# Optimization experiments

Measured on AMD Instinct MI355X. Metric: run time of the kernel, lower is better.

## Reference

```python
import jax, jax.numpy as jnp
import numpy as np

INPUT_DIM = 4096
BOTTLENECK = 32768
A = 2
K = 0.05
# eval-mode sparsity count: max(1, int(bottleneck * a * k))
K_COUNT = max(1, int(BOTTLENECK * A * K))  # 3276


def setup_inputs() -> dict:
    key = jax.random.key(0)
    kx, kw = jax.random.split(key)
    x = jax.random.normal(kx, (4096, INPUT_DIM), dtype=jnp.float32)
    # encoder weight [bottleneck, input_dim], like nn.Linear(input_dim, bottleneck)
    W = jax.random.normal(kw, (BOTTLENECK, INPUT_DIM), dtype=jnp.float32) * (1.0 / np.sqrt(INPUT_DIM))
    b_enc = jnp.zeros((BOTTLENECK,), dtype=jnp.float32)
    b_dec = jnp.zeros((INPUT_DIM,), dtype=jnp.float32)
    return {"x": x, "W": W, "b_enc": b_enc, "b_dec": b_dec, "epoch": 0}


def reference(x, W, b_enc, b_dec, epoch):
    # encode: z1 = x @ W^T + b_enc  -> [B, bottleneck]
    z1 = jnp.einsum("bi,hi->bh", x, W) + b_enc
    # eval-mode k-winner-take-all mask over dim 1
    _, topk_idx = jax.lax.top_k(z1, K_COUNT)  # [B, K_COUNT]
    rows = jnp.arange(z1.shape[0])[:, None]
    mask = jnp.zeros_like(z1).at[rows, topk_idx].set(1.0)
    a1 = z1 * mask
    # tied-weight decode: z2 = a1 @ W + b_dec -> [B, input_dim]
    z2 = jnp.einsum("bh,hi->bi", a1, W) + b_dec
    return z2
```

## Files before the change

### kernel.cpp

```cpp
#include <hip/hip_runtime.h>
#include <hip/hip_bf16.h>
#include <stdint.h>


#define DIM      4096
#define BATCH    4096
#define NROWS_W  32768
#define KCNT     3276
#define DELTA    0.0066f
#define ROWCAP   256
#define HCAP     64
#define CANDCAP  3584

typedef __bf16 bf16x8 __attribute__((ext_vector_type(8)));
typedef __bf16 bf16x4 __attribute__((ext_vector_type(4)));
typedef float  f32x4  __attribute__((ext_vector_type(4)));

__device__ __forceinline__ void gload_lds16(const void* g, void* l) {
  __builtin_amdgcn_global_load_lds(
      (const __attribute__((address_space(1))) void*)g,
      (__attribute__((address_space(3))) void*)l, 16, 0, 0);
}

__global__ void k_cvtx(const float* __restrict__ s, __bf16* __restrict__ hi, int n4) {
  int i = blockIdx.x * 256 + threadIdx.x;
  const int stride = gridDim.x * 256;
  for (; i < n4; i += stride) {
    f32x4 v = ((const f32x4*)s)[i];
    bf16x4 h;
#pragma unroll
    for (int j = 0; j < 4; ++j) h[j] = (__bf16)v[j];
    ((bf16x4*)hi)[i] = h;
  }
}

__global__ void k_splitw(const float* __restrict__ W, __bf16* __restrict__ Wh,
                         __bf16* __restrict__ Wt) {
  __shared__ __bf16 t[64][65];
  const int c0 = blockIdx.x * 64, r0 = blockIdx.y * 64;
  const int tx = threadIdx.x, ty = threadIdx.y;
  for (int rr = ty; rr < 64; rr += 8) {
    const float w = W[(long)(r0 + rr) * DIM + c0 + tx];
    const __bf16 h = (__bf16)w;
    Wh[(long)(r0 + rr) * DIM + c0 + tx] = h;
    t[rr][tx] = h;
  }
  __syncthreads();
  for (int cc = ty; cc < 64; cc += 8)
    Wt[(long)(c0 + cc) * NROWS_W + r0 + tx] = t[tx][cc];
}

__global__ __launch_bounds__(256, 2)
void k_gemm(const __bf16* __restrict__ A, const __bf16* __restrict__ B,
            const float* __restrict__ bias, float* __restrict__ C,
            int M, int N, int Kt) {
  constexpr int BM = 128, BN = 128, BK = 64;
  __shared__ __align__(16) __bf16 sA[BM * BK];
  __shared__ __align__(16) __bf16 sB[BN * BK];

  const int tid = threadIdx.x;
  const int nbn = N / BN;
  int bm, bn;
  if ((M / BM) % 16 == 0 && nbn % 32 == 0) {
    const int nsbn = nbn / 32;
    const int g = blockIdx.x >> 9, r = blockIdx.x & 511;
    bm = (g / nsbn) * 16 + (r >> 5);
    bn = (g % nsbn) * 32 + (r & 31);
  } else {
    bm = blockIdx.x / nbn;
    bn = blockIdx.x % nbn;
  }
  const int m0 = bm * BM, n0 = bn * BN;
  const int lane = tid & 63, wid = tid >> 6;
  const int wm = wid >> 1, wn = wid & 1;
  const int lr = lane & 15, lk = lane >> 4;
  const int swz = (lr & 7) << 4;

  f32x4 acc[4][4] = {};

  for (int k0 = 0; k0 < Kt; k0 += BK) {
#pragma unroll
    for (int r = 0; r < 4; ++r) {
      const int o = (r * 256 + tid) * 16;
      const int row = o >> 7;
      const int colb = (o & 127) ^ ((row & 7) << 4);
      const long gA = ((long)(m0 + row) * Kt + k0) * 2 + colb;
      const long gB = ((long)(n0 + row) * Kt + k0) * 2 + colb;
      gload_lds16((const char*)A + gA, (char*)sA + o);
      gload_lds16((const char*)B + gB, (char*)sB + o);
    }
    __syncthreads();

#pragma unroll
    for (int kk = 0; kk < 2; ++kk) {
      bf16x8 va[4], vb[4];
      const int kbase = (kk * 64 + lk * 16) ^ swz;
#pragma unroll
      for (int m = 0; m < 4; ++m) {
        const int row = wm * 64 + m * 16 + lr;
        va[m] = *(const bf16x8*)((const char*)sA + row * 128 + kbase);
      }
#pragma unroll
      for (int n = 0; n < 4; ++n) {
        const int row = wn * 64 + n * 16 + lr;
        vb[n] = *(const bf16x8*)((const char*)sB + row * 128 + kbase);
      }
#pragma unroll
      for (int m = 0; m < 4; ++m)
#pragma unroll
        for (int n = 0; n < 4; ++n)
          acc[m][n] = __builtin_amdgcn_mfma_f32_16x16x32_bf16(va[m], vb[n], acc[m][n], 0, 0, 0);
    }
    __syncthreads();
  }

#pragma unroll
  for (int n = 0; n < 4; ++n) {
    const int col = n0 + wn * 64 + n * 16 + lr;
    const float bv = bias[col];
#pragma unroll
    for (int m = 0; m < 4; ++m) {
      const int r0r = m0 + wm * 64 + m * 16 + lk * 4;
#pragma unroll
      for (int j = 0; j < 4; ++j)
        C[(long)(r0r + j) * N + col] = acc[m][n][j] + bv;
    }
  }
}

__device__ __forceinline__ unsigned f2o(float f) {
  unsigned b = __float_as_uint(f);
  return ((int)b < 0) ? ~b : (b | 0x80000000u);
}
__device__ __forceinline__ float o2f(unsigned u) {
  unsigned b = (u & 0x80000000u) ? (u & 0x7FFFFFFFu) : ~u;
  return __uint_as_float(b);
}

__global__ __launch_bounds__(256)
void k_topk4(const float* __restrict__ z1, float* __restrict__ thr,
             unsigned* __restrict__ rowlist, unsigned* __restrict__ rowcnt,
             unsigned* __restrict__ c1, unsigned* __restrict__ bucket,
             unsigned* __restrict__ bcnt, __bf16* __restrict__ a1, int kwant) {
  __shared__ unsigned hist[4096];
  __shared__ float cv[CANDCAP];
  __shared__ unsigned short ci[CANDCAP];
  __shared__ unsigned s_n, s_bin, s_rem, s_wt[4], s_cnt, s_above;
  const int tid = threadIdx.x;
  const int b = blockIdx.x;
  const f32x4* zv = (const f32x4*)(z1 + (long)b * NROWS_W);
  constexpr int NV = NROWS_W / 4;

#pragma unroll
  for (int j = 0; j < 16; ++j) hist[tid + j * 256] = 0;
  if (tid == 0) { s_n = 0; s_cnt = 0; s_above = 0; }
  __syncthreads();
  for (int i = tid; i < NV; i += 256) {
    f32x4 v = zv[i];
#pragma unroll
    for (int j = 0; j < 4; ++j) atomicAdd(&hist[f2o(v[j]) >> 20], 1u);
  }
  __syncthreads();
  unsigned p = 0;
#pragma unroll
  for (int j = 0; j < 16; ++j) p += hist[tid * 16 + j];
  unsigned sfx = p;
  const int lane = tid & 63, w = tid >> 6;
#pragma unroll
  for (int off = 1; off < 64; off <<= 1) {
    unsigned o = __shfl_down(sfx, off);
    sfx += (lane + off < 64) ? o : 0u;
  }
  if (lane == 0) s_wt[w] = sfx;
  __syncthreads();
  unsigned above_waves = 0;
  for (int ww = w + 1; ww < 4; ++ww) above_waves += s_wt[ww];
  const unsigned incl = sfx + above_waves;
  const int cnt = __syncthreads_count(incl >= (unsigned)kwant);
  const int tstar = cnt - 1;
  if (tid == tstar) {
    unsigned cum = incl - p;
    int bsel = tid * 16;
    for (int j = 15; j >= 0; --j) {
      const unsigned h = hist[tid * 16 + j];
      if (cum + h >= (unsigned)kwant) { bsel = tid * 16 + j; break; }
      cum += h;
    }
    s_bin = (unsigned)bsel;
    s_rem = (unsigned)kwant - cum;
  }
  __syncthreads();
  const unsigned binsel = s_bin;
  unsigned rem = s_rem;

  const unsigned blo = (binsel > 0) ? binsel - 1 : 0;
  const unsigned bhi = (binsel < 4095) ? binsel + 1 : 4095;
  for (int i = tid; i < NV; i += 256) {
    f32x4 v = zv[i];
#pragma unroll
    for (int j = 0; j < 4; ++j) {
      const unsigned bin = f2o(v[j]) >> 20;
      if (bin >= blo && bin <= bhi) {
        const unsigned jj = atomicAdd(&s_n, 1u);
        if (jj < CANDCAP) { cv[jj] = v[j]; ci[jj] = (unsigned short)(i * 4 + j); }
      }
    }
  }
  __syncthreads();
  const int n = (s_n < CANDCAP) ? (int)s_n : CANDCAP;

  unsigned pfx = 0;
#pragma unroll
  for (int pass = 0; pass < 3; ++pass) {
    const int shift = (pass == 0) ? 12 : (pass == 1) ? 4 : 0;
    const int nb = (pass == 2) ? 16 : 256;
    if (tid < 256) hist[tid] = 0;
    __syncthreads();
    for (int i = tid; i < n; i += 256) {
      const unsigned u = f2o(cv[i]);
      if ((u >> 20) != binsel) continue;
      const unsigned v = u & 0xFFFFFu;
      const bool m = (pass == 0) ? true
                     : (pass == 1) ? ((v >> 12) == (pfx >> 12))
                                   : ((v >> 4) == (pfx >> 4));
      if (m) atomicAdd(&hist[(v >> shift) & (nb - 1)], 1u);
    }
    __syncthreads();
    if (tid == 0) {
      unsigned cum = 0;
      int d = nb - 1;
      for (; d > 0; --d) {
        if (cum + hist[d] >= rem) break;
        cum += hist[d];
      }
      s_bin = (unsigned)d;
      s_rem = rem - cum;
    }
    __syncthreads();
    pfx |= (s_bin << shift);
    rem = s_rem;
    __syncthreads();
  }
  const float t = o2f((binsel << 20) | pfx);
  if (tid == 0) thr[b] = t;
  const float hi = t + DELTA, lo = t - DELTA;

  for (int i = tid; i < n; i += 256) {
    const float v = cv[i];
    if (v >= lo && v <= hi) {
      const unsigned idx = ci[i];
      const unsigned jj = atomicAdd(&s_cnt, 1u);
      if (jj < ROWCAP) {
        rowlist[(long)b * ROWCAP + jj] = idx;
        const unsigned pq = atomicAdd(&bcnt[idx], 1u);
        if (pq < HCAP) bucket[(long)idx * HCAP + pq] = ((unsigned)b << 9) | jj;
      }
    }
  }

  unsigned my_above = 0;
  bf16x4* av = (bf16x4*)(a1 + (long)b * NROWS_W);
  for (int i = tid; i < NV; i += 256) {
    f32x4 v = zv[i];
    bf16x4 o;
#pragma unroll
    for (int j = 0; j < 4; ++j) {
      const bool in = v[j] > hi;
      my_above += in ? 1u : 0u;
      o[j] = in ? (__bf16)v[j] : (__bf16)0.0f;
    }
    av[i] = o;
  }
  atomicAdd(&s_above, my_above);
  __syncthreads();
  if (tid == 0) {
    rowcnt[b] = (s_cnt < ROWCAP) ? s_cnt : ROWCAP;
    c1[b] = s_above;
  }
}

__global__ void k_zero(f32x4* __restrict__ p, int nvec) {
  int i = blockIdx.x * 256 + threadIdx.x;
  if (i < nvec) {
    f32x4 z = {0.f, 0.f, 0.f, 0.f};
    p[i] = z;
  }
}

__global__ void k_recompute(const float* __restrict__ W, const float* __restrict__ x,
                            const unsigned* __restrict__ bucket,
                            const unsigned* __restrict__ bcnt,
                            float* __restrict__ exact) {
  const int h = blockIdx.x;
  unsigned n = bcnt[h];
  if (n > HCAP) n = HCAP;
  if (n == 0) return;
  __shared__ float wrec[DIM];
  const long wb = (long)h * DIM;
  for (int i = threadIdx.x; i < DIM / 4; i += 256)
    ((f32x4*)wrec)[i] = ((const f32x4*)(W + wb))[i];
  __syncthreads();
  const int w = threadIdx.x >> 6, lane = threadIdx.x & 63;
  for (unsigned e = w; e < n; e += 4) {
    const unsigned ent = bucket[(long)h * HCAP + e];
    const int b = ent >> 9, j = ent & 511;
    const f32x4* xv = (const f32x4*)(x + (long)b * DIM);
    float s = 0.f;
#pragma unroll
    for (int c = 0; c < 16; ++c) {
      const int i4 = c * 64 + lane;
      f32x4 v = xv[i4];
      const float* wr = &wrec[i4 * 4];
#pragma unroll
      for (int q = 0; q < 4; ++q) s += v[q] * wr[q];
    }
#pragma unroll
    for (int m = 32; m; m >>= 1) s += __shfl_xor(s, m);
    if (lane == 0) exact[(long)b * ROWCAP + j] = s;
  }
}

__global__ void k_select(const float* __restrict__ exact, const unsigned* __restrict__ rowlist,
                         const unsigned* __restrict__ rowcnt, const unsigned* __restrict__ c1,
                         const float* __restrict__ z1, __bf16* __restrict__ a1) {
  const int b = blockIdx.x;
  const int n = (int)rowcnt[b];
  const int need = KCNT - (int)c1[b];
  __shared__ float vals[ROWCAP];
  const int j = threadIdx.x;
  vals[j] = (j < n) ? exact[(long)b * ROWCAP + j] : -1e30f;
  __syncthreads();
  if (j < n) {
    const float vj = vals[j];
    int rank = 0;
    for (int i = 0; i < n; ++i) {
      const float vi = vals[i];
      rank += (vi > vj || (vi == vj && i < j)) ? 1 : 0;
    }
    if (rank < need) {
      const unsigned h = rowlist[(long)b * ROWCAP + j];
      const long off = (long)b * NROWS_W + h;
      a1[off] = (__bf16)z1[off];
    }
  }
}

extern "C" void kernel_launch(void* const* d_in, const int* in_sizes, int n_in,
                              void* d_out, int out_size, void* d_ws, size_t ws_size,
                              hipStream_t stream) {
  const float* x     = (const float*)d_in[0];
  const float* W     = (const float*)d_in[1];
  const float* b_enc = (const float*)d_in[2];
  const float* b_dec = (const float*)d_in[3];
  float* out = (float*)d_out;

  const long NW = (long)NROWS_W * DIM;
  const long NX = (long)BATCH * DIM;
  const long NZ = (long)BATCH * NROWS_W;

  char* ws = (char*)d_ws;
  __bf16* Wh = (__bf16*)ws;
  __bf16* Wt = Wh + NW;
  __bf16* xh = Wt + NW;
  float*  z1 = (float*)(xh + NX);
  float*  thr = z1 + NZ;
  char*   sc = (char*)(thr + BATCH);
  unsigned* rowcnt  = (unsigned*)sc;
  unsigned* c1      = (unsigned*)(sc + 16384);
  unsigned* bcnt    = (unsigned*)(sc + 32768);
  float*    exact   = (float*)(sc + 163840);
  unsigned* rowlist = (unsigned*)(sc + 4358144);
  unsigned* bucket  = (unsigned*)(sc + 8552448);
  __bf16* a1 = Wh;

  const size_t needed = (size_t)(4 * NW + 2 * NX) + (size_t)4 * NZ + 4 * BATCH + 17000000;
  if (ws_size < needed) return;

  k_splitw<<<dim3(DIM / 64, NROWS_W / 64), dim3(64, 8), 0, stream>>>(W, Wh, Wt);
  k_cvtx<<<2048, 256, 0, stream>>>(x, xh, (int)(NX / 4));

  k_gemm<<<(BATCH / 128) * (NROWS_W / 128), 256, 0, stream>>>(
      xh, Wh, b_enc, z1, BATCH, NROWS_W, DIM);

  k_zero<<<32, 256, 0, stream>>>((f32x4*)bcnt, 131072 / 16);
  k_topk4<<<BATCH, 256, 0, stream>>>(z1, thr, rowlist, rowcnt, c1, bucket, bcnt, a1, KCNT);
  k_recompute<<<NROWS_W, 256, 0, stream>>>(W, x, bucket, bcnt, exact);
  k_select<<<BATCH, ROWCAP, 0, stream>>>(exact, rowlist, rowcnt, c1, z1, a1);

  k_gemm<<<(BATCH / 128) * (DIM / 128), 256, 0, stream>>>(
      a1, Wt, b_dec, out, BATCH, DIM, NROWS_W);
}
```

Before: 3.553 ms.

## Switch GEMM operands to fp16, narrow threshold band, fold bcnt zeroing

Converts the x and W copies, the sparse activation and both MFMA GEMMs from bf16 to fp16. fp16 keeps more mantissa bits, so the band of uncertain values around the top-k threshold shrinks from 0.0066 to 0.0025. That means fewer candidates go through the exact fp32 recompute and select kernels. The separate zeroing kernel for bcnt is folded into the weight split kernel, removing one launch. The risk is fp16 overflow or underflow on inputs outside this test's range, and a narrower band could misclassify borderline top-k elements.

```diff
diff --git a/kernel.cpp b/kernel.cpp
--- a/kernel.cpp
+++ b/kernel.cpp
@@ -7,14 +7,14 @@
 #define BATCH    4096
 #define NROWS_W  32768
 #define KCNT     3276
-#define DELTA    0.0066f
+#define DELTA    0.0025f
 #define ROWCAP   256
 #define HCAP     64
 #define CANDCAP  3584
 
-typedef __bf16 bf16x8 __attribute__((ext_vector_type(8)));
-typedef __bf16 bf16x4 __attribute__((ext_vector_type(4)));
-typedef float  f32x4  __attribute__((ext_vector_type(4)));
+typedef _Float16 f16x8 __attribute__((ext_vector_type(8)));
+typedef _Float16 f16x4 __attribute__((ext_vector_type(4)));
+typedef float    f32x4 __attribute__((ext_vector_type(4)));
 
 __device__ __forceinline__ void gload_lds16(const void* g, void* l) {
   __builtin_amdgcn_global_load_lds(
@@ -22,26 +22,33 @@
       (__attribute__((address_space(3))) void*)l, 16, 0, 0);
 }
 
-__global__ void k_cvtx(const float* __restrict__ s, __bf16* __restrict__ hi, int n4) {
+__global__ void k_cvtx(const float* __restrict__ s, _Float16* __restrict__ hi, int n4) {
   int i = blockIdx.x * 256 + threadIdx.x;
   const int stride = gridDim.x * 256;
   for (; i < n4; i += stride) {
     f32x4 v = ((const f32x4*)s)[i];
-    bf16x4 h;
-#pragma unroll
-    for (int j = 0; j < 4; ++j) h[j] = (__bf16)v[j];
-    ((bf16x4*)hi)[i] = h;
-  }
-}
-
-__global__ void k_splitw(const float* __restrict__ W, __bf16* __restrict__ Wh,
-                         __bf16* __restrict__ Wt) {
-  __shared__ __bf16 t[64][65];
+    f16x4 h;
+#pragma unroll
+    for (int j = 0; j < 4; ++j) h[j] = (_Float16)v[j];
+    ((f16x4*)hi)[i] = h;
+  }
+}
+
+__global__ void k_splitw(const float* __restrict__ W, _Float16* __restrict__ Wh,
+                         _Float16* __restrict__ Wt, f32x4* __restrict__ bcntv) {
+  __shared__ _Float16 t[64][65];
   const int c0 = blockIdx.x * 64, r0 = blockIdx.y * 64;
   const int tx = threadIdx.x, ty = threadIdx.y;
+  if (blockIdx.y == 0) {
+    const int idx = blockIdx.x * 512 + ty * 64 + tx;
+    if (idx < 8192) {
+      f32x4 z = {0.f, 0.f, 0.f, 0.f};
+      bcntv[idx] = z;
+    }
+  }
   for (int rr = ty; rr < 64; rr += 8) {
     const float w = W[(long)(r0 + rr) * DIM + c0 + tx];
-    const __bf16 h = (__bf16)w;
+    const _Float16 h = (_Float16)w;
     Wh[(long)(r0 + rr) * DIM + c0 + tx] = h;
     t[rr][tx] = h;
   }
@@ -51,12 +58,12 @@
 }
 
 __global__ __launch_bounds__(256, 2)
-void k_gemm(const __bf16* __restrict__ A, const __bf16* __restrict__ B,
+void k_gemm(const _Float16* __restrict__ A, const _Float16* __restrict__ B,
             const float* __restrict__ bias, float* __restrict__ C,
             int M, int N, int Kt) {
   constexpr int BM = 128, BN = 128, BK = 64;
-  __shared__ __align__(16) __bf16 sA[BM * BK];
-  __shared__ __align__(16) __bf16 sB[BN * BK];
+  __shared__ __align__(16) _Float16 sA[BM * BK];
+  __shared__ __align__(16) _Float16 sB[BN * BK];
 
   const int tid = threadIdx.x;
   const int nbn = N / BN;
@@ -93,23 +100,23 @@
 
 #pragma unroll
     for (int kk = 0; kk < 2; ++kk) {
-      bf16x8 va[4], vb[4];
+      f16x8 va[4], vb[4];
       const int kbase = (kk * 64 + lk * 16) ^ swz;
 #pragma unroll
       for (int m = 0; m < 4; ++m) {
         const int row = wm * 64 + m * 16 + lr;
-        va[m] = *(const bf16x8*)((const char*)sA + row * 128 + kbase);
+        va[m] = *(const f16x8*)((const char*)sA + row * 128 + kbase);
       }
 #pragma unroll
       for (int n = 0; n < 4; ++n) {
         const int row = wn * 64 + n * 16 + lr;
-        vb[n] = *(const bf16x8*)((const char*)sB + row * 128 + kbase);
+        vb[n] = *(const f16x8*)((const char*)sB + row * 128 + kbase);
       }
 #pragma unroll
       for (int m = 0; m < 4; ++m)
 #pragma unroll
         for (int n = 0; n < 4; ++n)
-          acc[m][n] = __builtin_amdgcn_mfma_f32_16x16x32_bf16(va[m], vb[n], acc[m][n], 0, 0, 0);
+          acc[m][n] = __builtin_amdgcn_mfma_f32_16x16x32_f16(va[m], vb[n], acc[m][n], 0, 0, 0);
     }
     __syncthreads();
   }
@@ -141,7 +148,7 @@
 void k_topk4(const float* __restrict__ z1, float* __restrict__ thr,
              unsigned* __restrict__ rowlist, unsigned* __restrict__ rowcnt,
              unsigned* __restrict__ c1, unsigned* __restrict__ bucket,
-             unsigned* __restrict__ bcnt, __bf16* __restrict__ a1, int kwant) {
+             unsigned* __restrict__ bcnt, _Float16* __restrict__ a1, int kwant) {
   __shared__ unsigned hist[4096];
   __shared__ float cv[CANDCAP];
   __shared__ unsigned short ci[CANDCAP];
@@ -259,15 +266,15 @@
   }
 
   unsigned my_above = 0;
-  bf16x4* av = (bf16x4*)(a1 + (long)b * NROWS_W);
+  f16x4* av = (f16x4*)(a1 + (long)b * NROWS_W);
   for (int i = tid; i < NV; i += 256) {
     f32x4 v = zv[i];
-    bf16x4 o;
+    f16x4 o;
 #pragma unroll
     for (int j = 0; j < 4; ++j) {
       const bool in = v[j] > hi;
       my_above += in ? 1u : 0u;
-      o[j] = in ? (__bf16)v[j] : (__bf16)0.0f;
+      o[j] = in ? (_Float16)v[j] : (_Float16)0.0f;
     }
     av[i] = o;
   }
@@ -276,14 +283,6 @@
   if (tid == 0) {
     rowcnt[b] = (s_cnt < ROWCAP) ? s_cnt : ROWCAP;
     c1[b] = s_above;
-  }
-}
-
-__global__ void k_zero(f32x4* __restrict__ p, int nvec) {
-  int i = blockIdx.x * 256 + threadIdx.x;
-  if (i < nvec) {
-    f32x4 z = {0.f, 0.f, 0.f, 0.f};
-    p[i] = z;
   }
 }
 
@@ -322,7 +321,7 @@
 
 __global__ void k_select(const float* __restrict__ exact, const unsigned* __restrict__ rowlist,
                          const unsigned* __restrict__ rowcnt, const unsigned* __restrict__ c1,
-                         const float* __restrict__ z1, __bf16* __restrict__ a1) {
+                         const float* __restrict__ z1, _Float16* __restrict__ a1) {
   const int b = blockIdx.x;
   const int n = (int)rowcnt[b];
   const int need = KCNT - (int)c1[b];
@@ -340,7 +339,7 @@
     if (rank < need) {
       const unsigned h = rowlist[(long)b * ROWCAP + j];
       const long off = (long)b * NROWS_W + h;
-      a1[off] = (__bf16)z1[off];
+      a1[off] = (_Float16)z1[off];
     }
   }
 }
@@ -359,9 +358,9 @@
   const long NZ = (long)BATCH * NROWS_W;
 
   char* ws = (char*)d_ws;
-  __bf16* Wh = (__bf16*)ws;
-  __bf16* Wt = Wh + NW;
-  __bf16* xh = Wt + NW;
+  _Float16* Wh = (_Float16*)ws;
+  _Float16* Wt = Wh + NW;
+  _Float16* xh = Wt + NW;
   float*  z1 = (float*)(xh + NX);
   float*  thr = z1 + NZ;
   char*   sc = (char*)(thr + BATCH);
@@ -371,18 +370,17 @@
   float*    exact   = (float*)(sc + 163840);
   unsigned* rowlist = (unsigned*)(sc + 4358144);
   unsigned* bucket  = (unsigned*)(sc + 8552448);
-  __bf16* a1 = Wh;
+  _Float16* a1 = Wh;
 
   const size_t needed = (size_t)(4 * NW + 2 * NX) + (size_t)4 * NZ + 4 * BATCH + 17000000;
   if (ws_size < needed) return;
 
-  k_splitw<<<dim3(DIM / 64, NROWS_W / 64), dim3(64, 8), 0, stream>>>(W, Wh, Wt);
+  k_splitw<<<dim3(DIM / 64, NROWS_W / 64), dim3(64, 8), 0, stream>>>(W, Wh, Wt, (f32x4*)bcnt);
   k_cvtx<<<2048, 256, 0, stream>>>(x, xh, (int)(NX / 4));
 
   k_gemm<<<(BATCH / 128) * (NROWS_W / 128), 256, 0, stream>>>(
       xh, Wh, b_enc, z1, BATCH, NROWS_W, DIM);
 
-  k_zero<<<32, 256, 0, stream>>>((f32x4*)bcnt, 131072 / 16);
   k_topk4<<<BATCH, 256, 0, stream>>>(z1, thr, rowlist, rowcnt, c1, bucket, bcnt, a1, KCNT);
   k_recompute<<<NROWS_W, 256, 0, stream>>>(W, x, bucket, bcnt, exact);
   k_select<<<BATCH, ROWCAP, 0, stream>>>(exact, rowlist, rowcnt, c1, z1, a1);
```

After: 3.154 ms. 11.2% less time.
